# Optimization experiments

Measured on AMD Instinct MI355X. Metric: run time of the kernel, lower is better.

## Reference

```python
import jax, jax.numpy as jnp
import numpy as np

NUM_TOKENS = 32000
DIM = 1024
DEPTH = 4
HEADS = 16
DIM_HEAD = 64
FF_MULT = 4
DH_FF = int(DIM * FF_MULT * 2 / 3)  # 2730
B, N = 2, 2048
ROPE_THETA = 10000.0


def setup_inputs() -> dict:
    key = jax.random.key(0)
    ks = jax.random.split(key, 8)
    s = 0.02
    return {
        "tokens": jax.random.randint(ks[0], (B, N), 0, NUM_TOKENS),
        "token_emb": jax.random.normal(ks[1], (NUM_TOKENS, DIM)) * s,
        "attn_norm_w": jnp.ones((DEPTH, DIM)),
        "wqkv": jax.random.normal(ks[2], (DEPTH, DIM, 3 * HEADS * DIM_HEAD)) * s,
        "wo": jax.random.normal(ks[3], (DEPTH, HEADS * DIM_HEAD, DIM)) * s,
        "ff_norm_w": jnp.ones((DEPTH, DIM)),
        "ff_w1": jax.random.normal(ks[4], (DEPTH, DIM, 2 * DH_FF)) * s,
        "ff_b1": jnp.zeros((DEPTH, 2 * DH_FF)),
        "ff_w2": jax.random.normal(ks[5], (DEPTH, DH_FF, DIM)) * s,
        "ff_b2": jnp.zeros((DEPTH, DIM)),
        "final_norm_w": jnp.ones((DIM,)),
        "logits_w": jax.random.normal(ks[6], (DIM, NUM_TOKENS)) * s,
        "logits_b": jnp.zeros((NUM_TOKENS,)),
    }


def rmsnorm(x, w):
    eps = jnp.finfo(x.dtype).eps  # torch RMSNorm default eps
    var = jnp.mean(jnp.square(x), axis=-1, keepdims=True)
    return x * jax.lax.rsqrt(var + eps) * w


def rotate_half(x):
    x1, x2 = jnp.split(x, 2, axis=-1)
    return jnp.concatenate((-x2, x1), axis=-1)


def apply_rope(pos, t):
    return t * jnp.cos(pos) + rotate_half(t) * jnp.sin(pos)


def reference(tokens, token_emb, attn_norm_w, wqkv, wo, ff_norm_w,
              ff_w1, ff_b1, ff_w2, ff_b2, final_norm_w, logits_w, logits_b):
    b, n = tokens.shape
    x = token_emb[tokens]  # [b, n, dim]

    # rotary embedding table [n, dim_head]
    inv_freq = ROPE_THETA ** (-(jnp.arange(0, DIM_HEAD, 2, dtype=jnp.float32) / DIM_HEAD))
    freqs = jnp.arange(n, dtype=jnp.float32)[:, None] * inv_freq[None, :]
    pos = jnp.concatenate((freqs, freqs), axis=-1)

    scale = DIM_HEAD ** -0.5
    causal = jnp.triu(jnp.ones((n, n), dtype=bool), 1)

    for l in range(DEPTH):
        # --- attention ---
        h = rmsnorm(x, attn_norm_w[l])
        qkv = jnp.einsum('bnd,de->bne', h, wqkv[l])
        qkv = qkv.reshape(b, n, 3, HEADS, DIM_HEAD)
        qkv = jnp.transpose(qkv, (2, 0, 3, 1, 4))  # [3, b, h, n, d]
        q, k, v = qkv[0], qkv[1], qkv[2]
        q = apply_rope(pos, q)
        k = apply_rope(pos, k)
        q = q * scale
        sim = jnp.einsum('bhid,bhjd->bhij', q, k)
        sim = jnp.where(causal, -jnp.finfo(sim.dtype).max, sim)
        attn = jax.nn.softmax(sim, axis=-1)
        out = jnp.einsum('bhij,bhjd->bhid', attn, v)
        out = jnp.transpose(out, (0, 2, 1, 3)).reshape(b, n, HEADS * DIM_HEAD)
        x = jnp.einsum('bne,ed->bnd', out, wo[l]) + x

        # --- GEGLU feedforward ---
        h = rmsnorm(x, ff_norm_w[l])
        u = jnp.einsum('bnd,de->bne', h, ff_w1[l]) + ff_b1[l]
        u1, gate = jnp.split(u, 2, axis=-1)
        g = jax.nn.gelu(gate, approximate=False) * u1
        x = jnp.einsum('bne,ed->bnd', g, ff_w2[l]) + ff_b2[l] + x

    embed = rmsnorm(x, final_norm_w)
    logits = jnp.einsum('bnd,dv->bnv', embed, logits_w) + logits_b
    return logits
```

## Files before the change

### kernel.cpp

```cpp
#include <hip/hip_runtime.h>
#include <math.h>
#include <stdint.h>


using short8v = __attribute__((ext_vector_type(8))) short;
using f32x4   = __attribute__((ext_vector_type(4))) float;

__device__ __forceinline__ float b2f(short s) {
    union { unsigned u; float f; } v; v.u = ((unsigned)(unsigned short)s) << 16; return v.f;
}
__device__ __forceinline__ short f2b(float f) {
    union { float f; unsigned u; } v; v.f = f;
    unsigned r = v.u + 0x7FFFu + ((v.u >> 16) & 1u);
    return (short)(r >> 16);
}

__device__ __forceinline__ void mfma_n(f32x4& d, short8v a, short8v b) {
    asm("v_mfma_f32_16x16x32_bf16 %0, %1, %2, %0" : "+v"(d) : "v"(a), "v"(b));
}
__device__ __forceinline__ void mfma_f(f32x4& d, short8v a, short8v b) {
    asm("s_nop 1\n\tv_mfma_f32_16x16x32_bf16 %0, %1, %2, %0" : "+v"(d) : "v"(a), "v"(b));
}
#define MFMA_FENCE() do { __builtin_amdgcn_sched_barrier(0); \
    asm volatile("s_nop 7\n\ts_nop 7"); \
    __builtin_amdgcn_sched_barrier(0); } while (0)

__device__ __forceinline__ void gload16(const void* g, void* l) {
    __builtin_amdgcn_global_load_lds(
        (const __attribute__((address_space(1))) unsigned int*)(uintptr_t)g,
        (__attribute__((address_space(3))) unsigned int*)(uintptr_t)l,
        16, 0, 0);
}

#define BARX() do { asm volatile("" ::: "memory"); \
    __builtin_amdgcn_s_barrier(); asm volatile("" ::: "memory"); } while (0)
#define VMN(n) asm volatile("s_waitcnt vmcnt(" #n ")" ::: "memory")
#define LGKM0() do { asm volatile("s_waitcnt lgkmcnt(0)" ::: "memory"); \
    __builtin_amdgcn_sched_barrier(0); } while (0)

__global__ void rope_table_k(float* __restrict__ ct, float* __restrict__ st) {
    int i = blockIdx.x * 256 + threadIdx.x;
    int n = i >> 5, j = i & 31;
    float freq = expf(-(float)j * (9.210340371976184f / 32.f));
    float a = (float)n * freq;
    ct[i] = cosf(a);
    st[i] = sinf(a);
}

__global__ void embed_k(const int* __restrict__ tok, const float* __restrict__ emb,
                        float* __restrict__ x) {
    int row = blockIdx.x;
    int tk = tok[row];
    const float4* src = (const float4*)(emb + (size_t)tk * 1024);
    float4* dst = (float4*)(x + (size_t)row * 1024);
    dst[threadIdx.x] = src[threadIdx.x];
}

__global__ void wconv_k(const float* __restrict__ W, short* __restrict__ T,
                        int K, int N, int Kpad,
                        size_t w_lstride, size_t t_lstride) {
    W += blockIdx.z * w_lstride;
    T += blockIdx.z * t_lstride;
    int n0 = blockIdx.x * 32, k0 = blockIdx.y * 32;
    __shared__ float tile[32][33];
    int t = threadIdx.x;
    int kk = t >> 3, ns = (t & 7) * 4;
    float4 v = make_float4(0.f, 0.f, 0.f, 0.f);
    int gk = k0 + kk;
    if (gk < K) {
        if (n0 + ns + 3 < N) {
            v = *(const float4*)(W + (size_t)gk * N + n0 + ns);
        } else {
            float tmp[4] = {0.f, 0.f, 0.f, 0.f};
            #pragma unroll
            for (int j = 0; j < 4; ++j)
                if (n0 + ns + j < N) tmp[j] = W[(size_t)gk * N + n0 + ns + j];
            v = make_float4(tmp[0], tmp[1], tmp[2], tmp[3]);
        }
    }
    tile[kk][ns + 0] = v.x; tile[kk][ns + 1] = v.y;
    tile[kk][ns + 2] = v.z; tile[kk][ns + 3] = v.w;
    __syncthreads();
    int nn = t >> 3, ks = (t & 7) * 4;
    short o[4];
    #pragma unroll
    for (int j = 0; j < 4; ++j) o[j] = f2b(tile[ks + j][nn]);
    *(int2*)(T + (size_t)(n0 + nn) * Kpad + k0 + ks) = *(int2*)o;
}

__global__ void rmsnorm_k(const float* __restrict__ x, const float* __restrict__ wt,
                          short* __restrict__ out) {
    int row = blockIdx.x;
    int t = threadIdx.x;
    const float* xr = x + (size_t)row * 1024;
    float4 v = ((const float4*)xr)[t];
    float ss = v.x * v.x + v.y * v.y + v.z * v.z + v.w * v.w;
    #pragma unroll
    for (int off = 32; off > 0; off >>= 1) ss += __shfl_down(ss, off, 64);
    __shared__ float red[4];
    if ((t & 63) == 0) red[t >> 6] = ss;
    __syncthreads();
    float tot = red[0] + red[1] + red[2] + red[3];
    float inv = rsqrtf(tot * (1.f / 1024.f) + 1.1920929e-7f);
    float4 wv = ((const float4*)wt)[t];
    int2 pk;
    pk.x = (int)(unsigned short)f2b(v.x * inv * wv.x) |
           ((int)(unsigned short)f2b(v.y * inv * wv.y) << 16);
    pk.y = (int)(unsigned short)f2b(v.z * inv * wv.z) |
           ((int)(unsigned short)f2b(v.w * inv * wv.w) << 16);
    *(int2*)(out + (size_t)row * 1024 + t * 4) = pk;
}

__global__ void geglu_k(const short* __restrict__ u, short* __restrict__ gbuf) {
    int r = blockIdx.x;
    int c8 = blockIdx.y * 256 + threadIdx.x;
    if (c8 >= 344) return;
    int c = c8 * 8;
    short o8[8];
    if (c + 8 <= 2730) {
        short8v u1 = *(const short8v*)(u + (size_t)r * 5460 + c);
        short8v gt = *(const short8v*)(u + (size_t)r * 5460 + 2730 + c);
        #pragma unroll
        for (int j = 0; j < 8; ++j) {
            float g = b2f(gt[j]);
            o8[j] = f2b(0.5f * g * (1.f + erff(g * 0.7071067811865475f)) * b2f(u1[j]));
        }
    } else {
        #pragma unroll
        for (int j = 0; j < 8; ++j) {
            int col = c + j;
            float v = 0.f;
            if (col < 2730) {
                float u1 = b2f(u[(size_t)r * 5460 + col]);
                float g  = b2f(u[(size_t)r * 5460 + 2730 + col]);
                v = 0.5f * g * (1.f + erff(g * 0.7071067811865475f)) * u1;
            }
            o8[j] = f2b(v);
        }
    }
    *(int4*)(gbuf + (size_t)r * 2752 + c) = *(int4*)o8;
}

template <bool BIAS, bool RES, bool OUTBF16>
__global__ __launch_bounds__(256, 4) void gemm2h(
    const short* __restrict__ A, const short* __restrict__ Bt,
    const float* __restrict__ bias, const float* __restrict__ res,
    void* __restrict__ outp, int N, int lda, int ldb, int ksteps) {
    __shared__ __align__(16) short As[64 * 32];
    __shared__ __align__(16) short Bs[128 * 32];
    const int t = threadIdx.x;
    const int lane = t & 63;
    const int w = t >> 6, wm = w >> 1, wn = w & 1;
    const int c = lane & 15, g = lane >> 4;

    const int nwg = (int)gridDim.x;
    const int cpx = nwg >> 3;
    const int wg = ((int)blockIdx.x & 7) * cpx + ((int)blockIdx.x >> 3);
    const int m0 = (wg & 63) << 6;
    const int n0 = (wg >> 6) << 7;

    const int srow = w * 16 + (lane >> 2);
    const int sseg = (lane & 3) * 8;
    const short* ga0 = A  + (size_t)(m0 + srow) * lda + sseg;
    const short* gb0 = Bt + (size_t)(n0 + w * 32 + (lane >> 2)) * ldb + sseg;
    const short* gb1 = Bt + (size_t)(n0 + w * 32 + 16 + (lane >> 2)) * ldb + sseg;
    short* la0 = &As[w * 512];
    short* lb0 = &Bs[(w * 2 + 0) * 512];
    short* lb1 = &Bs[(w * 2 + 1) * 512];

    f32x4 acc[2][4] = {};

    for (int kt = 0; kt < ksteps; ++kt) {
        const int k0 = kt << 5;
        __syncthreads();
        gload16(ga0 + k0, la0);
        gload16(gb0 + k0, lb0);
        gload16(gb1 + k0, lb1);
        __syncthreads();
        short8v af[2], bf[4];
        #pragma unroll
        for (int mi = 0; mi < 2; ++mi)
            af[mi] = *(const short8v*)&As[(wm * 32 + mi * 16 + c) * 32 + g * 8];
        #pragma unroll
        for (int ni = 0; ni < 4; ++ni)
            bf[ni] = *(const short8v*)&Bs[(wn * 64 + ni * 16 + c) * 32 + g * 8];
        #pragma unroll
        for (int mi = 0; mi < 2; ++mi)
            #pragma unroll
            for (int ni = 0; ni < 4; ++ni)
                mfma_n(acc[mi][ni], af[mi], bf[ni]);
    }
    MFMA_FENCE();
    #pragma unroll
    for (int mi = 0; mi < 2; ++mi) {
        #pragma unroll
        for (int ni = 0; ni < 4; ++ni) {
            int col = n0 + wn * 64 + ni * 16 + c;
            if (col < N) {
                float bv = BIAS ? bias[col] : 0.f;
                #pragma unroll
                for (int i = 0; i < 4; ++i) {
                    int row = m0 + wm * 32 + mi * 16 + g * 4 + i;
                    size_t off = (size_t)row * N + col;
                    float v = acc[mi][ni][i] + bv;
                    if (RES) v += res[off];
                    if (OUTBF16) ((short*)outp)[off] = f2b(v);
                    else         ((float*)outp)[off] = v;
                }
            }
        }
    }
}

template <bool BIAS, bool RES, bool OUTBF16, bool ROPE>
__global__ __launch_bounds__(512, 1) void gemm3(
    const short* __restrict__ A, const short* __restrict__ Bt,
    const float* __restrict__ bias, const float* __restrict__ res,
    void* __restrict__ outp, int N, int lda, int ldb, int nrowsB, int KT,
    const float* __restrict__ ct, const float* __restrict__ st,
    short* __restrict__ vtb) {
    __shared__ __align__(16) short L[49152];
    const int t = threadIdx.x;
    const int lane = t & 63;
    const int w = t >> 6;
    const int wm = w >> 2, wn = w & 3;
    const int c = lane & 15, g = lane >> 4;

    const int nwg = (int)gridDim.x, cpx = nwg >> 3;
    const int wg = ((int)blockIdx.x & 7) * cpx + ((int)blockIdx.x >> 3);
    const int m0 = (wg & 31) << 7;
    const int n0 = (wg >> 5) << 8;

    const int rS = t >> 3, sS = t & 7;
    const int sSw = (sS ^ (rS & 7)) << 3;
    size_t aoffh[2], broff[2][2];
    #pragma unroll
    for (int h = 0; h < 2; ++h)
        aoffh[h] = (size_t)(m0 + h * 64 + rS) * lda + sSw;
    #pragma unroll
    for (int h = 0; h < 2; ++h)
        #pragma unroll
        for (int i = 0; i < 2; ++i) {
            int brow = n0 + h * 128 + rS + i * 64;
            if (brow > nrowsB - 1) brow = nrowsB - 1;
            broff[h][i] = (size_t)brow * ldb + sSw;
        }
    short* ldsA[2][2];
    short* ldsB[2][2];
    #pragma unroll
    for (int p = 0; p < 2; ++p)
        #pragma unroll
        for (int h = 0; h < 2; ++h) {
            ldsA[p][h] = &L[(p * 2 + h) * 4096 + w * 512];
            ldsB[p][h] = &L[16384 + (p * 2 + h) * 8192 + w * 512];
        }

    const int cb0 = ((g * 8) ^ ((c & 7) * 8));
    const int vbA0 = wm * 4096 + c * 64 + cb0;
    const int vbA1 = vbA0 ^ 32;
    const int vbB0 = 16384 + (wn >> 1) * 8192 + (wn & 1) * 4096 + c * 64 + cb0;
    const int vbB1 = vbB0 ^ 32;

    #define STA3(p, h, kt) gload16(A + aoffh[h] + (kt) * 64, ldsA[p][h])
    #define STB3(p, h, kt) do { \
        gload16(Bt + broff[h][0] + (kt) * 64, ldsB[p][h]); \
        gload16(Bt + broff[h][1] + (kt) * 64, ldsB[p][h] + 4096); } while (0)
    #define LDA3(p, mi, ks) (*(const short8v*)&L[(p) * 8192 + (mi) * 1024 + ((ks) ? vbA1 : vbA0)])
    #define LDB3(p, ni, ks) (*(const short8v*)&L[(p) * 16384 + (ni) * 1024 + ((ks) ? vbB1 : vbB0)])
    #define MFMA8(MLO, NLO, BV) do { \
        _Pragma("unroll") for (int ks_ = 0; ks_ < 2; ++ks_) \
        _Pragma("unroll") for (int mi_ = 0; mi_ < 2; ++mi_) \
        _Pragma("unroll") for (int ni_ = 0; ni_ < 2; ++ni_) \
            mfma_n(acc[(MLO) + mi_][(NLO) + ni_], av[(MLO) + mi_][ks_], BV[(NLO) + ni_][ks_]); \
        } while (0)

    f32x4 acc[4][4] = {};
    short8v av[4][2], bc[4][2], bn[4][2];

    STB3(0, 1, 0); STB3(0, 0, 0); STA3(0, 0, 0); STA3(0, 1, 0);
    STB3(1, 1, 1); STB3(1, 0, 1); STA3(1, 0, 1); STA3(1, 1, 1);
    VMN(6);
    BARX();
    #pragma unroll
    for (int ni = 0; ni < 4; ++ni)
        #pragma unroll
        for (int ks = 0; ks < 2; ++ks)
            bc[ni][ks] = LDB3(0, ni, ks);
    LGKM0();
    BARX();
    asm volatile("s_nop 7\n\ts_nop 7");

    for (int KB = 0; KB < KT; KB += 2) {
        const bool st1 = (KB + 2 < KT);
        const bool st2 = (KB + 3 < KT);
        #pragma unroll
        for (int mi = 0; mi < 2; ++mi)
            #pragma unroll
            for (int ks = 0; ks < 2; ++ks) av[mi][ks] = LDA3(0, mi, ks);
        if (st1) STB3(0, 1, KB + 2);
        BARX();
        __builtin_amdgcn_s_setprio(1); MFMA8(0, 0, bc); __builtin_amdgcn_s_setprio(0);
        BARX();
        #pragma unroll
        for (int mi = 2; mi < 4; ++mi)
            #pragma unroll
            for (int ks = 0; ks < 2; ++ks) av[mi][ks] = LDA3(0, mi, ks);
        if (st1) { STB3(0, 0, KB + 2); VMN(6); } else { VMN(2); }
        BARX();
        __builtin_amdgcn_s_setprio(1); MFMA8(2, 0, bc); __builtin_amdgcn_s_setprio(0);
        BARX();
        #pragma unroll
        for (int ni = 0; ni < 2; ++ni)
            #pragma unroll
            for (int ks = 0; ks < 2; ++ks) bn[ni][ks] = LDB3(1, ni, ks);
        if (st1) STA3(0, 0, KB + 2);
        BARX();
        __builtin_amdgcn_s_setprio(1); MFMA8(0, 2, bc); __builtin_amdgcn_s_setprio(0);
        BARX();
        #pragma unroll
        for (int ni = 2; ni < 4; ++ni)
            #pragma unroll
            for (int ks = 0; ks < 2; ++ks) bn[ni][ks] = LDB3(1, ni, ks);
        if (st1) { STA3(0, 1, KB + 2); VMN(6); } else { VMN(0); }
        BARX();
        __builtin_amdgcn_s_setprio(1); MFMA8(2, 2, bc); __builtin_amdgcn_s_setprio(0);
        BARX();
        #pragma unroll
        for (int mi = 0; mi < 2; ++mi)
            #pragma unroll
            for (int ks = 0; ks < 2; ++ks) av[mi][ks] = LDA3(1, mi, ks);
        if (st2) STB3(1, 1, KB + 3);
        BARX();
        __builtin_amdgcn_s_setprio(1); MFMA8(0, 0, bn); __builtin_amdgcn_s_setprio(0);
        BARX();
        #pragma unroll
        for (int mi = 2; mi < 4; ++mi)
            #pragma unroll
            for (int ks = 0; ks < 2; ++ks) av[mi][ks] = LDA3(1, mi, ks);
        if (st2) STB3(1, 0, KB + 3);
        if (st1) VMN(6);
        BARX();
        __builtin_amdgcn_s_setprio(1); MFMA8(2, 0, bn); __builtin_amdgcn_s_setprio(0);
        BARX();
        if (st1) {
            #pragma unroll
            for (int ni = 0; ni < 2; ++ni)
                #pragma unroll
                for (int ks = 0; ks < 2; ++ks) bc[ni][ks] = LDB3(0, ni, ks);
        }
        if (st2) STA3(1, 0, KB + 3);
        BARX();
        __builtin_amdgcn_s_setprio(1); MFMA8(0, 2, bn); __builtin_amdgcn_s_setprio(0);
        BARX();
        if (st1) {
            #pragma unroll
            for (int ni = 2; ni < 4; ++ni)
                #pragma unroll
                for (int ks = 0; ks < 2; ++ks) bc[ni][ks] = LDB3(0, ni, ks);
        }
        if (st2) STA3(1, 1, KB + 3);
        if (st1) VMN(6);
        BARX();
        __builtin_amdgcn_s_setprio(1); MFMA8(2, 2, bn); __builtin_amdgcn_s_setprio(0);
        BARX();
    }

    MFMA_FENCE();

    if (ROPE) {
        const int colbase = n0 + wn * 64;
        const int sec = colbase >> 10;
        if (sec < 2) {
            const float sc = (sec == 0) ? 0.18033688011112042f : 1.0f;
            #pragma unroll
            for (int mi = 0; mi < 4; ++mi)
                #pragma unroll
                for (int ni = 0; ni < 2; ++ni) {
                    const int col = colbase + ni * 16 + c;
                    const int jj = ni * 16 + c;
                    #pragma unroll
                    for (int i = 0; i < 4; ++i) {
                        int row = m0 + wm * 64 + mi * 16 + g * 4 + i;
                        int n = row & 2047;
                        float cv = ct[n * 32 + jj], sv = st[n * 32 + jj];
                        float a = acc[mi][ni][i], b = acc[mi][ni + 2][i];
                        ((short*)outp)[(size_t)row * N + col]      = f2b((a * cv - b * sv) * sc);
                        ((short*)outp)[(size_t)row * N + col + 32] = f2b((b * cv + a * sv) * sc);
                    }
                }
        } else {
            const int h64 = (colbase - 2048) >> 6;
            #pragma unroll
            for (int mi = 0; mi < 4; ++mi) {
                const int r0 = m0 + wm * 64 + mi * 16 + g * 4;
                const int bb = r0 >> 11, nn = r0 & 2047;
                #pragma unroll
                for (int ni = 0; ni < 4; ++ni) {
                    const int d = ni * 16 + c;
                    short s4[4];
                    #pragma unroll
                    for (int i = 0; i < 4; ++i) s4[i] = f2b(acc[mi][ni][i]);
                    *(int2*)(vtb + (size_t)((bb * 16 + h64) * 64 + d) * 2048 + nn) =
                        *(int2*)s4;
                }
            }
        }
        return;
    }

    #pragma unroll
    for (int mi = 0; mi < 4; ++mi) {
        #pragma unroll
        for (int ni = 0; ni < 4; ++ni) {
            int col = n0 + wn * 64 + ni * 16 + c;
            if (col < N) {
                float bv = BIAS ? bias[col] : 0.f;
                #pragma unroll
                for (int i = 0; i < 4; ++i) {
                    int row = m0 + wm * 64 + mi * 16 + g * 4 + i;
                    size_t off = (size_t)row * N + col;
                    float v = acc[mi][ni][i] + bv;
                    if (RES) v += res[off];
                    if (OUTBF16) ((short*)outp)[off] = f2b(v);
                    else         ((float*)outp)[off] = v;
                }
            }
        }
    }
    #undef STA3
    #undef STB3
    #undef LDA3
    #undef LDB3
    #undef MFMA8
}

template <bool BIAS, bool RES, bool OUTBF16>
__global__ __launch_bounds__(512, 2) void gemm4(
    const short* __restrict__ A, const short* __restrict__ Bt,
    const float* __restrict__ bias, const float* __restrict__ res,
    void* __restrict__ outp, int N, int lda, int ldb, int nrowsB, int KT) {
    __shared__ __align__(16) short L[65536];
    const int t = threadIdx.x;
    const int lane = t & 63;
    const int w = t >> 6;
    const int wm = w >> 2, wn = w & 3;
    const int c = lane & 15, g = lane >> 4;

    const int nwg = (int)gridDim.x, cpx = nwg >> 3;
    const int wg = ((int)blockIdx.x & 7) * cpx + ((int)blockIdx.x >> 3);
    const int m0 = (wg & 15) << 8;
    const int n0 = (wg >> 4) << 8;

    const int sub0 = t & 63;
    const int seg0 = sub0 >> 4, r0 = sub0 & 15;
    const int slab0 = t >> 6, slab1 = slab0 + 8;
    const size_t aoff0 = (size_t)(m0 + slab0 * 16 + r0) * lda + seg0 * 8;
    const size_t aoff1 = (size_t)(m0 + slab1 * 16 + r0) * lda + seg0 * 8;
    int br0 = n0 + slab0 * 16 + r0; if (br0 > nrowsB - 1) br0 = nrowsB - 1;
    int br1 = n0 + slab1 * 16 + r0; if (br1 > nrowsB - 1) br1 = nrowsB - 1;
    const size_t boff0 = (size_t)br0 * ldb + seg0 * 8;
    const size_t boff1 = (size_t)br1 * ldb + seg0 * 8;

    char* Lb = (char*)L;
    const int rb = g * 256 + c * 16;

    #define STA4(p, kh, kt) do { \
        gload16(A + aoff0 + (kt) * 64 + (kh) * 32, Lb + ((p)*2+(kh))*16384 + w*1024); \
        gload16(A + aoff1 + (kt) * 64 + (kh) * 32, Lb + ((p)*2+(kh))*16384 + 8192 + w*1024); } while (0)
    #define STB4(p, kh, kt) do { \
        gload16(Bt + boff0 + (kt) * 64 + (kh) * 32, Lb + 65536 + ((p)*2+(kh))*16384 + w*1024); \
        gload16(Bt + boff1 + (kt) * 64 + (kh) * 32, Lb + 65536 + ((p)*2+(kh))*16384 + 8192 + w*1024); } while (0)
    #define LDA4(p, ks, mi) (*(const short8v*)(Lb + ((p)*2+(ks))*16384 + (wm*8+(mi))*1024 + rb))
    #define LDB4(p, ks, ni) (*(const short8v*)(Lb + 65536 + ((p)*2+(ks))*16384 + (wn*4+(ni))*1024 + rb))
    #define MFMAQ(MB) do { \
        _Pragma("unroll") for (int mi_ = 0; mi_ < 4; ++mi_) \
        _Pragma("unroll") for (int ni_ = 0; ni_ < 4; ++ni_) \
            mfma_n(acc[(MB) + mi_][ni_], av[mi_], bv[ni_]); } while (0)

    f32x4 acc[8][4] = {};
    short8v av[4], bv[4];

    STA4(0, 0, 0); STB4(0, 0, 0); STA4(0, 1, 0); STB4(0, 1, 0);
    VMN(4);
    BARX();
    asm volatile("s_nop 7\n\ts_nop 7");

    #define TILE4(p, pn, tc, stg2) do { \
        _Pragma("unroll") for (int mi = 0; mi < 4; ++mi) av[mi] = LDA4(p, 0, mi); \
        _Pragma("unroll") for (int ni = 0; ni < 4; ++ni) bv[ni] = LDB4(p, 0, ni); \
        if (stg2) STA4(pn, 0, (tc) + 1); \
        BARX(); \
        __builtin_amdgcn_s_setprio(1); MFMAQ(0); __builtin_amdgcn_s_setprio(0); \
        BARX(); \
        _Pragma("unroll") for (int mi = 0; mi < 4; ++mi) av[mi] = LDA4(p, 0, mi + 4); \
        if (stg2) { STB4(pn, 0, (tc) + 1); VMN(4); } else { VMN(0); } \
        BARX(); \
        __builtin_amdgcn_s_setprio(1); MFMAQ(4); __builtin_amdgcn_s_setprio(0); \
        BARX(); \
        _Pragma("unroll") for (int mi = 0; mi < 4; ++mi) av[mi] = LDA4(p, 1, mi); \
        _Pragma("unroll") for (int ni = 0; ni < 4; ++ni) bv[ni] = LDB4(p, 1, ni); \
        if (stg2) STA4(pn, 1, (tc) + 1); \
        BARX(); \
        __builtin_amdgcn_s_setprio(1); MFMAQ(0); __builtin_amdgcn_s_setprio(0); \
        BARX(); \
        _Pragma("unroll") for (int mi = 0; mi < 4; ++mi) av[mi] = LDA4(p, 1, mi + 4); \
        if (stg2) { STB4(pn, 1, (tc) + 1); VMN(4); } \
        BARX(); \
        __builtin_amdgcn_s_setprio(1); MFMAQ(4); __builtin_amdgcn_s_setprio(0); \
        BARX(); \
    } while (0)

    for (int kt = 0; kt < KT; kt += 2) {
        TILE4(0, 1, kt, true);
        TILE4(1, 0, kt + 1, (kt + 2 < KT));
    }
    #undef TILE4

    MFMA_FENCE();
    #pragma unroll
    for (int mi = 0; mi < 8; ++mi) {
        #pragma unroll
        for (int ni = 0; ni < 4; ++ni) {
            int col = n0 + wn * 64 + ni * 16 + c;
            if (col < N) {
                float bvv = BIAS ? bias[col] : 0.f;
                #pragma unroll
                for (int i = 0; i < 4; ++i) {
                    int row = m0 + wm * 128 + mi * 16 + g * 4 + i;
                    size_t off = (size_t)row * N + col;
                    float v = acc[mi][ni][i] + bvv;
                    if (RES) v += res[off];
                    if (OUTBF16) ((short*)outp)[off] = f2b(v);
                    else         ((float*)outp)[off] = v;
                }
            }
        }
    }
    #undef STA4
    #undef STB4
    #undef LDA4
    #undef LDB4
    #undef MFMAQ
}

__global__ __launch_bounds__(256, 2) void attn_fwd(
    const short* __restrict__ qkv, const short* __restrict__ vt,
    short* __restrict__ o) {
    const int id = blockIdx.x;
    const int bh = id & 31;
    const int qs = id >> 5;
    const int qt = (qs < 8) ? qs : 23 - qs;
    const int b = bh >> 4, h = bh & 15;
    const int t = threadIdx.x, lane = t & 63, w = t >> 6;
    const int c = lane & 15, g = lane >> 4;
    __shared__ __align__(16) short Ks[128 * 72];
    __shared__ __align__(16) short Vs[64 * 136];
    __shared__ __align__(16) short Ps[128 * 136];

    #pragma unroll
    for (int i = 0; i < 4; ++i) {
        int idx = t + i * 256, r = idx >> 3, seg = idx & 7;
        *(int4*)&Ps[r * 136 + seg * 8] =
            *(const int4*)(qkv + (size_t)(b * 2048 + qt * 128 + r) * 3072 + h * 64 + seg * 8);
    }
    __syncthreads();
    short8v qf[2][2];
    #pragma unroll
    for (int mi = 0; mi < 2; ++mi)
        #pragma unroll
        for (int kk = 0; kk < 2; ++kk)
            qf[mi][kk] = *(const short8v*)&Ps[(w * 32 + mi * 16 + c) * 136 + kk * 32 + g * 8];

    f32x4 oacc[2][4] = {};
    float mrow[2][4], lrow[2][4];
    #pragma unroll
    for (int mi = 0; mi < 2; ++mi)
        #pragma unroll
        for (int i = 0; i < 4; ++i) { mrow[mi][i] = -3.0e38f; lrow[mi][i] = 0.f; }

    for (int jt = 0; jt <= qt; ++jt) {
        __syncthreads();
        #pragma unroll
        for (int i = 0; i < 4; ++i) {
            int idx = t + i * 256, r = idx >> 3, seg = idx & 7;
            *(int4*)&Ks[r * 72 + seg * 8] =
                *(const int4*)(qkv + (size_t)(b * 2048 + jt * 128 + r) * 3072
                               + 1024 + h * 64 + seg * 8);
        }
        #pragma unroll
        for (int i = 0; i < 4; ++i) {
            int idx = t + i * 256, d = idx >> 4, seg = idx & 15;
            *(int4*)&Vs[d * 136 + seg * 8] =
                *(const int4*)(vt + (size_t)(bh * 64 + d) * 2048 + jt * 128 + seg * 8);
        }
        __syncthreads();
        f32x4 sacc[2][8] = {};
        #pragma unroll
        for (int kk = 0; kk < 2; ++kk) {
            short8v kf[8];
            #pragma unroll
            for (int ni = 0; ni < 8; ++ni)
                kf[ni] = *(const short8v*)&Ks[(ni * 16 + c) * 72 + kk * 32 + g * 8];
            #pragma unroll
            for (int mi = 0; mi < 2; ++mi)
                #pragma unroll
                for (int ni = 0; ni < 8; ++ni) {
                    if (kk == 0) mfma_f(sacc[mi][ni], qf[mi][kk], kf[ni]);
                    else         mfma_n(sacc[mi][ni], qf[mi][kk], kf[ni]);
                }
        }
        MFMA_FENCE();
        if (jt == qt) {
            #pragma unroll
            for (int mi = 0; mi < 2; ++mi)
                #pragma unroll
                for (int ni = 0; ni < 8; ++ni)
                    #pragma unroll
                    for (int i = 0; i < 4; ++i) {
                        int qrow = w * 32 + mi * 16 + g * 4 + i;
                        int kcol = ni * 16 + c;
                        if (kcol > qrow) sacc[mi][ni][i] = -3.0e38f;
                    }
        }
        #pragma unroll
        for (int mi = 0; mi < 2; ++mi) {
            #pragma unroll
            for (int i = 0; i < 4; ++i) {
                float mx = sacc[mi][0][i];
                #pragma unroll
                for (int ni = 1; ni < 8; ++ni) mx = fmaxf(mx, sacc[mi][ni][i]);
                #pragma unroll
                for (int off = 1; off < 16; off <<= 1) mx = fmaxf(mx, __shfl_xor(mx, off, 64));
                float mnew = fmaxf(mrow[mi][i], mx);
                float alpha = __builtin_amdgcn_exp2f(mrow[mi][i] - mnew);
                mrow[mi][i] = mnew;
                float ls = 0.f;
                #pragma unroll
                for (int ni = 0; ni < 8; ++ni) {
                    float p = __builtin_amdgcn_exp2f(sacc[mi][ni][i] - mnew);
                    sacc[mi][ni][i] = p;
                    ls += p;
                }
                #pragma unroll
                for (int off = 1; off < 16; off <<= 1) ls += __shfl_xor(ls, off, 64);
                lrow[mi][i] = lrow[mi][i] * alpha + ls;
                #pragma unroll
                for (int df = 0; df < 4; ++df) oacc[mi][df][i] *= alpha;
            }
        }
        #pragma unroll
        for (int mi = 0; mi < 2; ++mi)
            #pragma unroll
            for (int ni = 0; ni < 8; ++ni)
                #pragma unroll
                for (int i = 0; i < 4; ++i)
                    Ps[(w * 32 + mi * 16 + g * 4 + i) * 136 + ni * 16 + c] =
                        f2b(sacc[mi][ni][i]);
        #pragma unroll
        for (int kk = 0; kk < 4; ++kk) {
            short8v pf[2], vf[4];
            #pragma unroll
            for (int mi = 0; mi < 2; ++mi)
                pf[mi] = *(const short8v*)&Ps[(w * 32 + mi * 16 + c) * 136 + kk * 32 + g * 8];
            #pragma unroll
            for (int df = 0; df < 4; ++df)
                vf[df] = *(const short8v*)&Vs[(df * 16 + c) * 136 + kk * 32 + g * 8];
            #pragma unroll
            for (int mi = 0; mi < 2; ++mi)
                #pragma unroll
                for (int df = 0; df < 4; ++df) {
                    if (kk == 0) mfma_f(oacc[mi][df], pf[mi], vf[df]);
                    else         mfma_n(oacc[mi][df], pf[mi], vf[df]);
                }
        }
    }
    MFMA_FENCE();
    #pragma unroll
    for (int mi = 0; mi < 2; ++mi)
        #pragma unroll
        for (int df = 0; df < 4; ++df)
            #pragma unroll
            for (int i = 0; i < 4; ++i) {
                int qrow = qt * 128 + w * 32 + mi * 16 + g * 4 + i;
                float v = oacc[mi][df][i] / lrow[mi][i];
                o[(size_t)(b * 2048 + qrow) * 1024 + h * 64 + df * 16 + c] = f2b(v);
            }
}

extern "C" void kernel_launch(void* const* d_in, const int* in_sizes, int n_in,
                              void* d_out, int out_size, void* d_ws, size_t ws_size,
                              hipStream_t stream) {
    (void)in_sizes; (void)n_in; (void)out_size; (void)ws_size;
    const int*   tokens = (const int*)d_in[0];
    const float* temb   = (const float*)d_in[1];
    const float* anw    = (const float*)d_in[2];
    const float* wqkv   = (const float*)d_in[3];
    const float* wo     = (const float*)d_in[4];
    const float* fnw    = (const float*)d_in[5];
    const float* fw1    = (const float*)d_in[6];
    const float* fb1    = (const float*)d_in[7];
    const float* fw2    = (const float*)d_in[8];
    const float* fb2    = (const float*)d_in[9];
    const float* finw   = (const float*)d_in[10];
    const float* lw     = (const float*)d_in[11];
    const float* lb     = (const float*)d_in[12];

    char* ws = (char*)d_ws;
    float* x    = (float*)(ws + 0);
    short* hb   = (short*)(ws + 16777216);
    short* qkv  = (short*)(ws + 25165824);
    short* ao   = (short*)(ws + 50331648);
    short* ub   = (short*)(ws + 58720256);
    short* gb   = (short*)(ws + 103448576);
    short* vtb  = (short*)(ws + 125992960);
    float* ct   = (float*)(ws + 134381568);
    float* st   = (float*)(ws + 134643712);
    short* qkvT = (short*)(ws + 134905856);
    short* woT  = (short*)(ws + 160071680);
    short* fw1T = (short*)(ws + 168460288);
    short* fw2T = (short*)(ws + 213549056);
    short* logT = (short*)(ws + 236093440);

    rope_table_k<<<256, 256, 0, stream>>>(ct, st);
    embed_k<<<4096, 256, 0, stream>>>(tokens, temb, x);

    wconv_k<<<dim3(96, 32, 4), 256, 0, stream>>>(
        wqkv, qkvT, 1024, 3072, 1024, (size_t)1024 * 3072, (size_t)3072 * 1024);
    wconv_k<<<dim3(32, 32, 4), 256, 0, stream>>>(
        wo, woT, 1024, 1024, 1024, (size_t)1024 * 1024, (size_t)1024 * 1024);
    wconv_k<<<dim3(172, 32, 4), 256, 0, stream>>>(
        fw1, fw1T, 1024, 5460, 1024, (size_t)1024 * 5460, (size_t)5504 * 1024);
    wconv_k<<<dim3(32, 86, 4), 256, 0, stream>>>(
        fw2, fw2T, 2730, 1024, 2752, (size_t)2730 * 1024, (size_t)1024 * 2752);
    wconv_k<<<dim3(1000, 32, 1), 256, 0, stream>>>(
        lw, logT, 1024, 32000, 1024, 0, 0);

    for (int l = 0; l < 4; ++l) {
        rmsnorm_k<<<4096, 256, 0, stream>>>(x, anw + l * 1024, hb);
        gemm3<false, false, true, true><<<32 * 12, 512, 0, stream>>>(
            hb, qkvT + (size_t)l * 3072 * 1024, nullptr, nullptr, qkv,
            3072, 1024, 1024, 3072, 16, ct, st, vtb);
        attn_fwd<<<512, 256, 0, stream>>>(qkv, vtb, ao);
        gemm2h<false, true, false><<<512, 256, 0, stream>>>(
            ao, woT + (size_t)l * 1024 * 1024, nullptr, x, x, 1024, 1024, 1024, 32);
        rmsnorm_k<<<4096, 256, 0, stream>>>(x, fnw + l * 1024, hb);
        gemm3<true, false, true, false><<<32 * 22, 512, 0, stream>>>(
            hb, fw1T + (size_t)l * 5504 * 1024, fb1 + l * 5460, nullptr, ub,
            5460, 1024, 1024, 5504, 16, nullptr, nullptr, nullptr);
        geglu_k<<<dim3(4096, 2), 256, 0, stream>>>(ub, gb);
        gemm2h<true, true, false><<<512, 256, 0, stream>>>(
            gb, fw2T + (size_t)l * 1024 * 2752, fb2 + l * 1024, x, x, 1024, 2752, 2752, 86);
    }
    rmsnorm_k<<<4096, 256, 0, stream>>>(x, finw, hb);
    gemm4<true, false, false><<<2000, 512, 0, stream>>>(
        hb, logT, lb, nullptr, d_out, 32000, 1024, 1024, 32000, 16);
}
```

Baseline: 1.797 ms.

## Fuse GEGLU into FF1 GEMM epilogue via interleaved weight layout

Reorders the converted FF1 weight rows so value and gate columns alternate in 16-column groups. The FF1 GEMM epilogue can then compute bias + GELU(gate)*value directly and write the padded 2752-wide gated buffer. This removes the separate geglu kernel and the round trip of the 5460-wide intermediate through memory. The trade-off is a heavier epilogue with erff calls in the GEMM, plus scattered 2-byte stores.

```diff
diff --git a/kernel.cpp b/kernel.cpp
--- a/kernel.cpp
+++ b/kernel.cpp
@@ -58,7 +58,7 @@
 
 __global__ void wconv_k(const float* __restrict__ W, short* __restrict__ T,
                         int K, int N, int Kpad,
-                        size_t w_lstride, size_t t_lstride) {
+                        size_t w_lstride, size_t t_lstride, int ilv) {
     W += blockIdx.z * w_lstride;
     T += blockIdx.z * t_lstride;
     int n0 = blockIdx.x * 32, k0 = blockIdx.y * 32;
@@ -85,7 +85,13 @@
     short o[4];
     #pragma unroll
     for (int j = 0; j < 4; ++j) o[j] = f2b(tile[ks + j][nn]);
-    *(int2*)(T + (size_t)(n0 + nn) * Kpad + k0 + ks) = *(int2*)o;
+    int oc = n0 + nn;
+    int dr = oc;
+    if (ilv) {
+        if (oc < 2730) dr = ((oc >> 4) << 5) + (oc & 15);
+        else { int jj = oc - 2730; dr = ((jj >> 4) << 5) + 16 + (jj & 15); }
+    }
+    *(int2*)(T + (size_t)dr * Kpad + k0 + ks) = *(int2*)o;
 }
 
 __global__ void rmsnorm_k(const float* __restrict__ x, const float* __restrict__ wt,
@@ -111,36 +117,6 @@
     *(int2*)(out + (size_t)row * 1024 + t * 4) = pk;
 }
 
-__global__ void geglu_k(const short* __restrict__ u, short* __restrict__ gbuf) {
-    int r = blockIdx.x;
-    int c8 = blockIdx.y * 256 + threadIdx.x;
-    if (c8 >= 344) return;
-    int c = c8 * 8;
-    short o8[8];
-    if (c + 8 <= 2730) {
-        short8v u1 = *(const short8v*)(u + (size_t)r * 5460 + c);
-        short8v gt = *(const short8v*)(u + (size_t)r * 5460 + 2730 + c);
-        #pragma unroll
-        for (int j = 0; j < 8; ++j) {
-            float g = b2f(gt[j]);
-            o8[j] = f2b(0.5f * g * (1.f + erff(g * 0.7071067811865475f)) * b2f(u1[j]));
-        }
-    } else {
-        #pragma unroll
-        for (int j = 0; j < 8; ++j) {
-            int col = c + j;
-            float v = 0.f;
-            if (col < 2730) {
-                float u1 = b2f(u[(size_t)r * 5460 + col]);
-                float g  = b2f(u[(size_t)r * 5460 + 2730 + col]);
-                v = 0.5f * g * (1.f + erff(g * 0.7071067811865475f)) * u1;
-            }
-            o8[j] = f2b(v);
-        }
-    }
-    *(int4*)(gbuf + (size_t)r * 2752 + c) = *(int4*)o8;
-}
-
 template <bool BIAS, bool RES, bool OUTBF16>
 __global__ __launch_bounds__(256, 4) void gemm2h(
     const short* __restrict__ A, const short* __restrict__ Bt,
@@ -212,7 +188,7 @@
     }
 }
 
-template <bool BIAS, bool RES, bool OUTBF16, bool ROPE>
+template <bool BIAS, bool RES, bool OUTBF16, int EPI>
 __global__ __launch_bounds__(512, 1) void gemm3(
     const short* __restrict__ A, const short* __restrict__ Bt,
     const float* __restrict__ bias, const float* __restrict__ res,
@@ -367,7 +343,7 @@
 
     MFMA_FENCE();
 
-    if (ROPE) {
+    if (EPI == 1) {
         const int colbase = n0 + wn * 64;
         const int sec = colbase >> 10;
         if (sec < 2) {
@@ -403,6 +379,36 @@
                     *(int2*)(vtb + (size_t)((bb * 16 + h64) * 64 + d) * 2048 + nn) =
                         *(int2*)s4;
                 }
+            }
+        }
+        return;
+    }
+
+    if (EPI == 2) {
+        const int colbase = n0 + wn * 64;
+        #pragma unroll
+        for (int np = 0; np < 2; ++np) {
+            const int j = ((colbase >> 5) + np) * 16 + c;
+            if (j < 2730) {
+                const float bu = bias[j], bg = bias[2730 + j];
+                #pragma unroll
+                for (int mi = 0; mi < 4; ++mi)
+                    #pragma unroll
+                    for (int i = 0; i < 4; ++i) {
+                        int row = m0 + wm * 64 + mi * 16 + g * 4 + i;
+                        float u1v = acc[mi][2 * np][i] + bu;
+                        float gv  = acc[mi][2 * np + 1][i] + bg;
+                        float val = 0.5f * gv * (1.f + erff(gv * 0.7071067811865475f)) * u1v;
+                        ((short*)outp)[(size_t)row * 2752 + j] = f2b(val);
+                    }
+            } else if (j < 2752) {
+                #pragma unroll
+                for (int mi = 0; mi < 4; ++mi)
+                    #pragma unroll
+                    for (int i = 0; i < 4; ++i) {
+                        int row = m0 + wm * 64 + mi * 16 + g * 4 + i;
+                        ((short*)outp)[(size_t)row * 2752 + j] = 0;
+                    }
             }
         }
         return;
@@ -710,7 +716,6 @@
     short* hb   = (short*)(ws + 16777216);
     short* qkv  = (short*)(ws + 25165824);
     short* ao   = (short*)(ws + 50331648);
-    short* ub   = (short*)(ws + 58720256);
     short* gb   = (short*)(ws + 103448576);
     short* vtb  = (short*)(ws + 125992960);
     float* ct   = (float*)(ws + 134381568);
@@ -718,36 +723,35 @@
     short* qkvT = (short*)(ws + 134905856);
     short* woT  = (short*)(ws + 160071680);
     short* fw1T = (short*)(ws + 168460288);
-    short* fw2T = (short*)(ws + 213549056);
-    short* logT = (short*)(ws + 236093440);
+    short* fw2T = (short*)(ws + 214597632);
+    short* logT = (short*)(ws + 237142016);
 
     rope_table_k<<<256, 256, 0, stream>>>(ct, st);
     embed_k<<<4096, 256, 0, stream>>>(tokens, temb, x);
 
     wconv_k<<<dim3(96, 32, 4), 256, 0, stream>>>(
-        wqkv, qkvT, 1024, 3072, 1024, (size_t)1024 * 3072, (size_t)3072 * 1024);
+        wqkv, qkvT, 1024, 3072, 1024, (size_t)1024 * 3072, (size_t)3072 * 1024, 0);
     wconv_k<<<dim3(32, 32, 4), 256, 0, stream>>>(
-        wo, woT, 1024, 1024, 1024, (size_t)1024 * 1024, (size_t)1024 * 1024);
-    wconv_k<<<dim3(172, 32, 4), 256, 0, stream>>>(
-        fw1, fw1T, 1024, 5460, 1024, (size_t)1024 * 5460, (size_t)5504 * 1024);
+        wo, woT, 1024, 1024, 1024, (size_t)1024 * 1024, (size_t)1024 * 1024, 0);
+    wconv_k<<<dim3(171, 32, 4), 256, 0, stream>>>(
+        fw1, fw1T, 1024, 5460, 1024, (size_t)1024 * 5460, (size_t)5632 * 1024, 1);
     wconv_k<<<dim3(32, 86, 4), 256, 0, stream>>>(
-        fw2, fw2T, 2730, 1024, 2752, (size_t)2730 * 1024, (size_t)1024 * 2752);
+        fw2, fw2T, 2730, 1024, 2752, (size_t)2730 * 1024, (size_t)1024 * 2752, 0);
     wconv_k<<<dim3(1000, 32, 1), 256, 0, stream>>>(
-        lw, logT, 1024, 32000, 1024, 0, 0);
+        lw, logT, 1024, 32000, 1024, 0, 0, 0);
 
     for (int l = 0; l < 4; ++l) {
         rmsnorm_k<<<4096, 256, 0, stream>>>(x, anw + l * 1024, hb);
-        gemm3<false, false, true, true><<<32 * 12, 512, 0, stream>>>(
+        gemm3<false, false, true, 1><<<32 * 12, 512, 0, stream>>>(
             hb, qkvT + (size_t)l * 3072 * 1024, nullptr, nullptr, qkv,
             3072, 1024, 1024, 3072, 16, ct, st, vtb);
         attn_fwd<<<512, 256, 0, stream>>>(qkv, vtb, ao);
         gemm2h<false, true, false><<<512, 256, 0, stream>>>(
             ao, woT + (size_t)l * 1024 * 1024, nullptr, x, x, 1024, 1024, 1024, 32);
         rmsnorm_k<<<4096, 256, 0, stream>>>(x, fnw + l * 1024, hb);
-        gemm3<true, false, true, false><<<32 * 22, 512, 0, stream>>>(
-            hb, fw1T + (size_t)l * 5504 * 1024, fb1 + l * 5460, nullptr, ub,
-            5460, 1024, 1024, 5504, 16, nullptr, nullptr, nullptr);
-        geglu_k<<<dim3(4096, 2), 256, 0, stream>>>(ub, gb);
+        gemm3<false, false, true, 2><<<32 * 22, 512, 0, stream>>>(
+            hb, fw1T + (size_t)l * 5632 * 1024, fb1 + l * 5460, nullptr, gb,
+            2752, 1024, 1024, 5632, 16, nullptr, nullptr, nullptr);
         gemm2h<true, true, false><<<512, 256, 0, stream>>>(
             gb, fw2T + (size_t)l * 1024 * 2752, fb2 + l * 1024, x, x, 1024, 2752, 2752, 86);
     }
```

New measurement: 1.740 ms, median of 2. 1.03x faster.
